# Performance work log

Hardware: AMD Instinct MI355X
Metric: run time of the kernel (lower is better)

Reference implementation:

```python
import jax, jax.numpy as jnp
import numpy as np

N = 100000        # nodes
E = 3200000       # edges (avg degree 32)
F_IN = 512        # input node features
HIDDEN = 16       # hardcoded in GCN.__init__
NUM_CLASSES = 40


def setup_inputs() -> dict:
    key = jax.random.key(0)
    k1, k2, k3, k4 = jax.random.split(key, 4)
    edge_index = jax.random.randint(k1, (2, E), 0, N, dtype=jnp.int32)
    x = jax.random.normal(k2, (N, F_IN), dtype=jnp.float32)
    # GCNConv weights (glorot-ish scale) and biases
    W1 = jax.random.normal(k3, (F_IN, HIDDEN), dtype=jnp.float32) * (1.0 / np.sqrt(F_IN))
    b1 = jnp.zeros((HIDDEN,), dtype=jnp.float32)
    W2 = jax.random.normal(k4, (HIDDEN, NUM_CLASSES), dtype=jnp.float32) * (1.0 / np.sqrt(HIDDEN))
    b2 = jnp.zeros((NUM_CLASSES,), dtype=jnp.float32)
    return {"edge_index": edge_index, "x": x, "W1": W1, "b1": b1, "W2": W2, "b2": b2}


def _gcn_conv(x, src, dst, W, b, n):
    # PyG GCNConv: linear transform, symmetric-normalized scatter-add aggregation
    h = x @ W                                             # [N, out]
    deg = jax.ops.segment_sum(jnp.ones_like(dst, dtype=h.dtype), dst, num_segments=n)
    dinv = jnp.where(deg > 0, jax.lax.rsqrt(deg), 0.0)    # deg^{-1/2}
    norm = dinv[src] * dinv[dst]                          # [E_total]
    out = jax.ops.segment_sum(h[src] * norm[:, None], dst, num_segments=n)
    return out + b


def reference(edge_index, x, W1, b1, W2, b2):
    n = x.shape[0]
    # GCNConv adds self-loops by default
    loop = jnp.arange(n, dtype=edge_index.dtype)
    src = jnp.concatenate([edge_index[0], loop])
    dst = jnp.concatenate([edge_index[1], loop])
    h = _gcn_conv(x, src, dst, W1, b1, n)
    h = jax.nn.relu(h)
    # F.dropout(training=self.training) -> identity in eval mode
    h = _gcn_conv(h, src, dst, W2, b2, n)
    return jax.nn.log_softmax(h, axis=1)[::20]
```

## Files before the change

kernel.cpp:

```cpp
#include <hip/hip_runtime.h>
#include <cstdint>
#include <math.h>

#define F_IN 512
#define HID  16
#define NCLS 40
#define OUT_STRIDE 20
#define TB   128
#define NBA  512

typedef __attribute__((ext_vector_type(8))) short short8;
typedef __attribute__((ext_vector_type(4))) float f32x4;

__device__ inline unsigned short f2bf(float f) {
    unsigned u = __float_as_uint(f);
    u += 0x7fff + ((u >> 16) & 1);
    return (unsigned short)(u >> 16);
}
__device__ inline float bf2f(unsigned short h) {
    return __uint_as_float(((unsigned)h) << 16);
}

__global__ __launch_bounds__(256) void k_a1(const int* __restrict__ dst,
                                            int* __restrict__ cnt,
                                            int E, int NB, int chunk) {
    __shared__ int h[1024];
    int t = threadIdx.x;
    for (int b = t; b < NB; b += 256) h[b] = 0;
    __syncthreads();
    int e0 = blockIdx.x * chunk, e1 = min(E, e0 + chunk);
    for (int e = e0 + t; e < e1; e += 256) {
        int d = __builtin_nontemporal_load(&dst[e]);
        atomicAdd(&h[d >> 7], 1);
    }
    __syncthreads();
    for (int b = t; b < NB; b += 256) cnt[(size_t)blockIdx.x * NB + b] = h[b];
}

__global__ __launch_bounds__(NBA) void k_a2a(const int* __restrict__ cnt,
                                             int* __restrict__ offsT,
                                             int* __restrict__ total, int NB) {
    __shared__ int s[NBA];
    int t = threadIdx.x, b = blockIdx.x;
    int v = cnt[(size_t)t * NB + b];
    s[t] = v;
    __syncthreads();
    for (int off = 1; off < NBA; off <<= 1) {
        int tmp = (t >= off) ? s[t - off] : 0;
        __syncthreads();
        s[t] += tmp;
        __syncthreads();
    }
    offsT[(size_t)b * NBA + t] = s[t] - v;
    if (t == NBA - 1) total[b] = s[t];
}

__global__ void k_a2b(const int* __restrict__ total, int* __restrict__ base, int NB) {
    __shared__ int s[1024];
    int t = threadIdx.x;
    int v = (t < NB) ? total[t] : 0;
    s[t] = v;
    __syncthreads();
    for (int off = 1; off < 1024; off <<= 1) {
        int tmp = (t >= off) ? s[t - off] : 0;
        __syncthreads();
        s[t] += tmp;
        __syncthreads();
    }
    if (t < NB) base[t] = s[t] - v;
    if (t == NB - 1) base[NB] = s[t];
}

__global__ __launch_bounds__(256) void k_a3(const int* __restrict__ src,
                                            const int* __restrict__ dst,
                                            const int* __restrict__ offsT,
                                            const int* __restrict__ base,
                                            unsigned* __restrict__ bin,
                                            int E, int NB, int chunk) {
    __shared__ int pos[1024];
    int t = threadIdx.x, blk = blockIdx.x;
    for (int b = t; b < NB; b += 256) pos[b] = base[b] + offsT[(size_t)b * NBA + blk];
    __syncthreads();
    int e0 = blk * chunk, e1 = min(E, e0 + chunk);
    for (int e = e0 + t; e < e1; e += 256) {
        int d = __builtin_nontemporal_load(&dst[e]);
        int s = __builtin_nontemporal_load(&src[e]);
        int p = atomicAdd(&pos[d >> 7], 1);
        bin[p] = ((unsigned)s << 7) | (unsigned)(d & (TB - 1));
    }
}

__global__ __launch_bounds__(256) void k_sortb(const unsigned* __restrict__ bin,
                                               const int* __restrict__ base,
                                               int* __restrict__ csr,
                                               int* __restrict__ roff,
                                               float* __restrict__ dinv, int N) {
    __shared__ int cnt[TB], incl[TB], pos[TB];
    int t = threadIdx.x, b = blockIdx.x;
    if (t < TB) cnt[t] = 0;
    __syncthreads();
    int j0 = base[b], j1 = base[b + 1];
    for (int j = j0 + t; j < j1; j += 256)
        atomicAdd(&cnt[bin[j] & (TB - 1)], 1);
    __syncthreads();
    if (t < TB) incl[t] = cnt[t];
    __syncthreads();
    for (int off = 1; off < TB; off <<= 1) {
        int v = (t < TB && t >= off) ? incl[t - off] : 0;
        __syncthreads();
        if (t < TB) incl[t] += v;
        __syncthreads();
    }
    if (t < TB) {
        int ex = incl[t] - cnt[t];
        pos[t] = ex;
        int node = b * TB + t;
        if (node < N) {
            roff[node] = j0 + ex;
            dinv[node] = rsqrtf((float)cnt[t] + 1.0f);
        } else if (node == N) {
            roff[N] = j0 + ex;
        }
    }
    __syncthreads();
    for (int j = j0 + t; j < j1; j += 256) {
        unsigned v = bin[j];
        int p = atomicAdd(&pos[v & (TB - 1)], 1);
        csr[j0 + p] = (int)(v >> 7);
    }
}

__global__ void k_prew(const float* __restrict__ W1, uint4* __restrict__ bfragg) {
    int idx = blockIdx.x * blockDim.x + threadIdx.x;
    if (idx >= 16 * 64) return;
    int kstep = idx >> 6, ln = idx & 63;
    int col = ln & 15, k0 = kstep * 32 + (ln >> 4) * 8;
    unsigned up[4];
#pragma unroll
    for (int i = 0; i < 4; i++) {
        float a = W1[(k0 + 2 * i) * HID + col];
        float b = W1[(k0 + 2 * i + 1) * HID + col];
        up[i] = (unsigned)f2bf(a) | ((unsigned)f2bf(b) << 16);
    }
    bfragg[idx] = make_uint4(up[0], up[1], up[2], up[3]);
}

__global__ __launch_bounds__(64) void k_gemm1m(const float* __restrict__ x,
                                               const uint4* __restrict__ bfragg,
                                               const float* __restrict__ dinv,
                                               unsigned short* __restrict__ h1b, int n) {
    int lane = threadIdx.x;
    int rows0 = blockIdx.x * 64;
    int arow = lane & 15, kgrp = lane >> 4;

    const float* xr[4];
#pragma unroll
    for (int rt = 0; rt < 4; rt++) {
        int r = rows0 + rt * 16 + arow;
        if (r >= n) r = n - 1;
        xr[rt] = x + (size_t)r * F_IN + kgrp * 8;
    }

    f32x4 acc[4];
#pragma unroll
    for (int rt = 0; rt < 4; rt++) acc[rt] = (f32x4){0.f, 0.f, 0.f, 0.f};

#pragma unroll 4
    for (int kstep = 0; kstep < 16; kstep++) {
        uint4 braw = bfragg[kstep * 64 + lane];
        short8 b;
        *(uint4*)&b = braw;
#pragma unroll
        for (int rt = 0; rt < 4; rt++) {
            float4 lo = *(const float4*)(xr[rt] + kstep * 32);
            float4 hi = *(const float4*)(xr[rt] + kstep * 32 + 4);
            short8 a;
            a[0] = (short)f2bf(lo.x); a[1] = (short)f2bf(lo.y);
            a[2] = (short)f2bf(lo.z); a[3] = (short)f2bf(lo.w);
            a[4] = (short)f2bf(hi.x); a[5] = (short)f2bf(hi.y);
            a[6] = (short)f2bf(hi.z); a[7] = (short)f2bf(hi.w);
            acc[rt] = __builtin_amdgcn_mfma_f32_16x16x32_bf16(a, b, acc[rt], 0, 0, 0);
        }
    }

    int col = lane & 15, rbase = (lane >> 4) * 4;
#pragma unroll
    for (int rt = 0; rt < 4; rt++) {
#pragma unroll
        for (int r = 0; r < 4; r++) {
            int row = rows0 + rt * 16 + rbase + r;
            if (row < n)
                h1b[(size_t)row * HID + col] = f2bf(acc[rt][r] * dinv[row]);
        }
    }
}

__global__ __launch_bounds__(256) void k_agg(const unsigned* __restrict__ h1u,
                                             const int* __restrict__ csr,
                                             const int* __restrict__ roff,
                                             const float* __restrict__ dinv,
                                             const float* __restrict__ b1,
                                             unsigned* __restrict__ zu, int n) {
    int lane = threadIdx.x & 63;
    int node = (blockIdx.x * blockDim.x + threadIdx.x) >> 6;
    if (node >= n) return;
    int cp = lane & 7;
    int sub = lane >> 3;
    int s0 = roff[node], s1 = roff[node + 1];
    float sa = 0.f, sb = 0.f;
    for (int j = s0 + sub; j < s1; j += 8) {
        unsigned u = h1u[(size_t)csr[j] * 8 + cp];
        sa += bf2f((unsigned short)(u & 0xffff));
        sb += bf2f((unsigned short)(u >> 16));
    }
    sa += __shfl_xor(sa, 8);  sb += __shfl_xor(sb, 8);
    sa += __shfl_xor(sa, 16); sb += __shfl_xor(sb, 16);
    sa += __shfl_xor(sa, 32); sb += __shfl_xor(sb, 32);
    unsigned us = h1u[(size_t)node * 8 + cp];
    sa += bf2f((unsigned short)(us & 0xffff));
    sb += bf2f((unsigned short)(us >> 16));
    float dv = dinv[node];
    float pa = dv * sa + b1[2 * cp];
    float pb = dv * sb + b1[2 * cp + 1];
    if (lane < 8) {
        unsigned short za = f2bf(fmaxf(pa, 0.f) * dv);
        unsigned short zbv = f2bf(fmaxf(pb, 0.f) * dv);
        zu[(size_t)node * 8 + cp] = (unsigned)za | ((unsigned)zbv << 16);
    }
}

__global__ void k_out(const unsigned short* __restrict__ zb,
                      const int* __restrict__ csr, const int* __restrict__ roff,
                      const float* __restrict__ dinv, const float* __restrict__ W2,
                      const float* __restrict__ b2, float* __restrict__ out, int nOut) {
    int lane = threadIdx.x & 63;
    int wv = (blockIdx.x * blockDim.x + threadIdx.x) >> 6;
    if (wv >= nOut) return;
    int node = wv * OUT_STRIDE;
    int c = lane & 15, sub = lane >> 4;
    int s0 = roff[node], s1 = roff[node + 1];
    float sum = 0.f;
    for (int j = s0 + sub; j < s1; j += 4)
        sum += bf2f(zb[(size_t)csr[j] * HID + c]);
    sum += __shfl_xor(sum, 16);
    sum += __shfl_xor(sum, 32);
    sum += bf2f(zb[(size_t)node * HID + c]);
    float a = dinv[node] * sum;

    int jj = lane < NCLS ? lane : 0;
    float v = 0.f;
#pragma unroll
    for (int cc = 0; cc < 16; cc++) {
        float ac = __shfl(a, cc);
        v = fmaf(ac, W2[cc * NCLS + jj], v);
    }
    v += b2[jj];

    float vm = lane < NCLS ? v : -INFINITY;
    for (int off = 1; off < 64; off <<= 1) vm = fmaxf(vm, __shfl_xor(vm, off));
    float ex = lane < NCLS ? expf(v - vm) : 0.f;
    float se = ex;
    for (int off = 1; off < 64; off <<= 1) se += __shfl_xor(se, off);
    float ls = logf(se);
    if (lane < NCLS) out[(size_t)wv * NCLS + lane] = v - vm - ls;
}

extern "C" void kernel_launch(void* const* d_in, const int* in_sizes, int n_in,
                              void* d_out, int out_size, void* d_ws, size_t ws_size,
                              hipStream_t stream) {
    const int E = in_sizes[0] / 2;
    const int N = in_sizes[1] / F_IN;
    const int nOut = (N + OUT_STRIDE - 1) / OUT_STRIDE;
    const int NB = (N + TB - 1) / TB;
    const int chunk = (E + NBA - 1) / NBA;

    const int* src = (const int*)d_in[0];
    const int* dst = src + E;
    const float* x  = (const float*)d_in[1];
    const float* W1 = (const float*)d_in[2];
    const float* b1 = (const float*)d_in[3];
    const float* W2 = (const float*)d_in[4];
    const float* b2 = (const float*)d_in[5];
    float* out = (float*)d_out;

    uint8_t* w = (uint8_t*)d_ws;
    size_t off = 0;
    auto carve = [&](size_t bytes) {
        void* p = w + off;
        off += (bytes + 15) & ~(size_t)15;
        return p;
    };
    float*          dinv  = (float*)carve((size_t)N * 4);
    unsigned*       bin   = (unsigned*)carve((size_t)E * 4);
    int*            cnt   = (int*)carve((size_t)NBA * NB * 4);
    int*            offsT = (int*)carve((size_t)NB * NBA * 4);
    int*            total = (int*)carve((size_t)NB * 4);
    int*            base  = (int*)carve((size_t)(NB + 1) * 4);
    int*            csr   = (int*)carve((size_t)E * 4);
    int*            roff  = (int*)carve((size_t)(N + 1) * 4);
    unsigned short* h1b   = (unsigned short*)carve((size_t)N * HID * 2);
    unsigned short* zb    = (unsigned short*)carve((size_t)N * HID * 2);
    uint4*          bfragg= (uint4*)carve((size_t)16 * 64 * 16);
    (void)ws_size; (void)n_in; (void)out_size;

    k_a1   <<<NBA, 256, 0, stream>>>(dst, cnt, E, NB, chunk);
    k_a2a  <<<NB, NBA, 0, stream>>>(cnt, offsT, total, NB);
    k_a2b  <<<1, 1024, 0, stream>>>(total, base, NB);
    k_a3   <<<NBA, 256, 0, stream>>>(src, dst, offsT, base, bin, E, NB, chunk);
    k_sortb<<<NB, 256, 0, stream>>>(bin, base, csr, roff, dinv, N);
    k_prew <<<16, 64, 0, stream>>>(W1, bfragg);
    k_gemm1m<<<(N + 63) / 64, 64, 0, stream>>>(x, bfragg, dinv, h1b, N);
    k_agg  <<<(N * 64 + 255) / 256, 256, 0, stream>>>((const unsigned*)h1b, csr, roff,
                                                      dinv, b1, (unsigned*)zb, N);
    k_out  <<<(nOut * 64 + 255) / 256, 256, 0, stream>>>(zb, csr, roff, dinv, W2, b2, out, nOut);
}
```

Measured before the change: 201.4 us.

## Widen CSR bucket size, fold W1 fragment prep into scan kernel, prefetch CSR indices

Doubles the per-bucket node count used for the two-level counting sort to 256 and halves the number of partition blocks to 256. This shrinks the histogram and offset arrays and lets the local sort kernel use all threads without guards. The W1 bf16 fragment packing moves into the single-block scan kernel, removing one launch. The aggregation loop now software-prefetches the next CSR index so the neighbour gather overlaps the index load. Larger buckets mean more shared-memory atomic contention per bucket.

```diff
diff --git a/kernel.cpp b/kernel.cpp
--- a/kernel.cpp
+++ b/kernel.cpp
@@ -6,8 +6,8 @@
 #define HID  16
 #define NCLS 40
 #define OUT_STRIDE 20
-#define TB   128
-#define NBA  512
+#define TB   256
+#define NBA  256
 
 typedef __attribute__((ext_vector_type(8))) short short8;
 typedef __attribute__((ext_vector_type(4))) float f32x4;
@@ -24,14 +24,14 @@
 __global__ __launch_bounds__(256) void k_a1(const int* __restrict__ dst,
                                             int* __restrict__ cnt,
                                             int E, int NB, int chunk) {
-    __shared__ int h[1024];
+    __shared__ int h[512];
     int t = threadIdx.x;
     for (int b = t; b < NB; b += 256) h[b] = 0;
     __syncthreads();
     int e0 = blockIdx.x * chunk, e1 = min(E, e0 + chunk);
     for (int e = e0 + t; e < e1; e += 256) {
         int d = __builtin_nontemporal_load(&dst[e]);
-        atomicAdd(&h[d >> 7], 1);
+        atomicAdd(&h[d >> 8], 1);
     }
     __syncthreads();
     for (int b = t; b < NB; b += 256) cnt[(size_t)blockIdx.x * NB + b] = h[b];
@@ -55,7 +55,8 @@
     if (t == NBA - 1) total[b] = s[t];
 }
 
-__global__ void k_a2b(const int* __restrict__ total, int* __restrict__ base, int NB) {
+__global__ void k_a2bw(const int* __restrict__ total, int* __restrict__ base, int NB,
+                       const float* __restrict__ W1, uint4* __restrict__ bfragg) {
     __shared__ int s[1024];
     int t = threadIdx.x;
     int v = (t < NB) ? total[t] : 0;
@@ -69,6 +70,17 @@
     }
     if (t < NB) base[t] = s[t] - v;
     if (t == NB - 1) base[NB] = s[t];
+
+    int kstep = t >> 6, ln = t & 63;
+    int col = ln & 15, k0 = kstep * 32 + (ln >> 4) * 8;
+    unsigned up[4];
+#pragma unroll
+    for (int i = 0; i < 4; i++) {
+        float a = W1[(k0 + 2 * i) * HID + col];
+        float b = W1[(k0 + 2 * i + 1) * HID + col];
+        up[i] = (unsigned)f2bf(a) | ((unsigned)f2bf(b) << 16);
+    }
+    bfragg[t] = make_uint4(up[0], up[1], up[2], up[3]);
 }
 
 __global__ __launch_bounds__(256) void k_a3(const int* __restrict__ src,
@@ -77,7 +89,7 @@
                                             const int* __restrict__ base,
                                             unsigned* __restrict__ bin,
                                             int E, int NB, int chunk) {
-    __shared__ int pos[1024];
+    __shared__ int pos[512];
     int t = threadIdx.x, blk = blockIdx.x;
     for (int b = t; b < NB; b += 256) pos[b] = base[b] + offsT[(size_t)b * NBA + blk];
     __syncthreads();
@@ -85,8 +97,8 @@
     for (int e = e0 + t; e < e1; e += 256) {
         int d = __builtin_nontemporal_load(&dst[e]);
         int s = __builtin_nontemporal_load(&src[e]);
-        int p = atomicAdd(&pos[d >> 7], 1);
-        bin[p] = ((unsigned)s << 7) | (unsigned)(d & (TB - 1));
+        int p = atomicAdd(&pos[d >> 8], 1);
+        bin[p] = ((unsigned)s << 8) | (unsigned)(d & (TB - 1));
     }
 }
 
@@ -97,52 +109,35 @@
                                                float* __restrict__ dinv, int N) {
     __shared__ int cnt[TB], incl[TB], pos[TB];
     int t = threadIdx.x, b = blockIdx.x;
-    if (t < TB) cnt[t] = 0;
+    cnt[t] = 0;
     __syncthreads();
     int j0 = base[b], j1 = base[b + 1];
     for (int j = j0 + t; j < j1; j += 256)
         atomicAdd(&cnt[bin[j] & (TB - 1)], 1);
     __syncthreads();
-    if (t < TB) incl[t] = cnt[t];
+    incl[t] = cnt[t];
     __syncthreads();
     for (int off = 1; off < TB; off <<= 1) {
-        int v = (t < TB && t >= off) ? incl[t - off] : 0;
-        __syncthreads();
-        if (t < TB) incl[t] += v;
-        __syncthreads();
-    }
-    if (t < TB) {
-        int ex = incl[t] - cnt[t];
-        pos[t] = ex;
-        int node = b * TB + t;
-        if (node < N) {
-            roff[node] = j0 + ex;
-            dinv[node] = rsqrtf((float)cnt[t] + 1.0f);
-        } else if (node == N) {
-            roff[N] = j0 + ex;
-        }
+        int v = (t >= off) ? incl[t - off] : 0;
+        __syncthreads();
+        incl[t] += v;
+        __syncthreads();
+    }
+    int ex = incl[t] - cnt[t];
+    pos[t] = ex;
+    int node = b * TB + t;
+    if (node < N) {
+        roff[node] = j0 + ex;
+        dinv[node] = rsqrtf((float)cnt[t] + 1.0f);
+    } else if (node == N) {
+        roff[N] = j0 + ex;
     }
     __syncthreads();
     for (int j = j0 + t; j < j1; j += 256) {
         unsigned v = bin[j];
         int p = atomicAdd(&pos[v & (TB - 1)], 1);
-        csr[j0 + p] = (int)(v >> 7);
-    }
-}
-
-__global__ void k_prew(const float* __restrict__ W1, uint4* __restrict__ bfragg) {
-    int idx = blockIdx.x * blockDim.x + threadIdx.x;
-    if (idx >= 16 * 64) return;
-    int kstep = idx >> 6, ln = idx & 63;
-    int col = ln & 15, k0 = kstep * 32 + (ln >> 4) * 8;
-    unsigned up[4];
-#pragma unroll
-    for (int i = 0; i < 4; i++) {
-        float a = W1[(k0 + 2 * i) * HID + col];
-        float b = W1[(k0 + 2 * i + 1) * HID + col];
-        up[i] = (unsigned)f2bf(a) | ((unsigned)f2bf(b) << 16);
-    }
-    bfragg[idx] = make_uint4(up[0], up[1], up[2], up[3]);
+        csr[j0 + p] = (int)(v >> 8);
+    }
 }
 
 __global__ __launch_bounds__(64) void k_gemm1m(const float* __restrict__ x,
@@ -208,8 +203,13 @@
     int sub = lane >> 3;
     int s0 = roff[node], s1 = roff[node + 1];
     float sa = 0.f, sb = 0.f;
-    for (int j = s0 + sub; j < s1; j += 8) {
-        unsigned u = h1u[(size_t)csr[j] * 8 + cp];
+    int j = s0 + sub;
+    int nxt = (j < s1) ? csr[j] : 0;
+    for (; j < s1; j += 8) {
+        int cur = nxt;
+        int jn = j + 8;
+        if (jn < s1) nxt = csr[jn];
+        unsigned u = h1u[(size_t)cur * 8 + cp];
         sa += bf2f((unsigned short)(u & 0xffff));
         sb += bf2f((unsigned short)(u >> 16));
     }
@@ -305,10 +305,9 @@
 
     k_a1   <<<NBA, 256, 0, stream>>>(dst, cnt, E, NB, chunk);
     k_a2a  <<<NB, NBA, 0, stream>>>(cnt, offsT, total, NB);
-    k_a2b  <<<1, 1024, 0, stream>>>(total, base, NB);
+    k_a2bw <<<1, 1024, 0, stream>>>(total, base, NB, W1, bfragg);
     k_a3   <<<NBA, 256, 0, stream>>>(src, dst, offsT, base, bin, E, NB, chunk);
-    k_sortb<<<NB, 256, 0, stream>>>(bin, base, csr, roff, dinv, N);
-    k_prew <<<16, 64, 0, stream>>>(W1, bfragg);
+    k_sortb<<<NB, TB, 0, stream>>>(bin, base, csr, roff, dinv, N);
     k_gemm1m<<<(N + 63) / 64, 64, 0, stream>>>(x, bfragg, dinv, h1b, N);
     k_agg  <<<(N * 64 + 255) / 256, 256, 0, stream>>>((const unsigned*)h1b, csr, roff,
                                                       dinv, b1, (unsigned*)zb, N);
```

New measurement: 182.9 us. 1.1x faster.
